# Optimization experiments

Measured on AMD Instinct MI355X. Metric: run time of the kernel, lower is better.

The kernel has to match this reference:

```python
import jax, jax.numpy as jnp
import numpy as np
from jax import lax

NUM_ITER = 40


def _pool(x, win, op, init):
    pads = [(0, 0), (0, 0)] + [(w // 2, w // 2) for w in win]
    return lax.reduce_window(x, init, op, (1, 1) + win, (1, 1, 1, 1, 1), pads)


def soft_erode(x):
    # -maxpool(-x) with zero-effect padding == min-pool padded with +inf.
    inf = jnp.asarray(jnp.inf, x.dtype)
    p1 = _pool(x, (3, 1, 1), lax.min, inf)
    p2 = _pool(x, (1, 3, 1), lax.min, inf)
    p3 = _pool(x, (1, 1, 3), lax.min, inf)
    return jnp.minimum(jnp.minimum(p1, p2), p3)


def soft_dilate(x):
    return _pool(x, (3, 3, 3), lax.max, jnp.asarray(-jnp.inf, x.dtype))


def soft_open(x):
    return soft_dilate(soft_erode(x))


def setup_inputs() -> dict:
    key = jax.random.key(0)
    img = jax.random.uniform(key, (2, 1, 192, 192, 192), dtype=jnp.float32)
    return {"img": img}


def reference(img):
    skeleton = jax.nn.relu(img - soft_open(img))

    def body(_, carry):
        im, skel = carry
        im = soft_erode(im)
        delta = jax.nn.relu(im - soft_open(im))
        skel = skel + jax.nn.relu(delta - skel * delta)
        return (im, skel)

    _, skeleton = lax.fori_loop(0, NUM_ITER, body, (img, skeleton))
    return skeleton
```

## Files before the change

### kernel.cpp

```cpp
#include <hip/hip_runtime.h>


#define Dn 192
#define Hn 192
#define Wn 192
#define PLANE (Hn * Wn)
#define TOTAL_ELEMS (2 * Dn * Hn * Wn)
#define NYG (Hn / 4)
#define ZPT 8
#define ZC (Dn / ZPT)
#define NBLK (NYG * ZC * 2)
#define NITER (ZPT + 4)

typedef _Float16 h2 __attribute__((ext_vector_type(2)));
typedef _Float16 h4 __attribute__((ext_vector_type(4)));

static __device__ __forceinline__ h2 h2min(h2 a, h2 b) { return __builtin_elementwise_min(a, b); }
static __device__ __forceinline__ h2 h2max(h2 a, h2 b) { return __builtin_elementwise_max(a, b); }
static __device__ __forceinline__ unsigned int u32(h2 v) { return __builtin_bit_cast(unsigned int, v); }
static __device__ __forceinline__ h2 h2c(unsigned int v) { return __builtin_bit_cast(h2, v); }

template <int CHUNK>
__device__ __forceinline__ int swizzle(int bid) {
    return (bid & 7) * CHUNK + (bid >> 3);
}

template <bool FIRST, bool LAST>
__global__ __launch_bounds__(192, 4) void step_k(const void* __restrict__ X_,
                                                 const _Float16* Sin,
                                                 void* Sout_,
                                                 _Float16* __restrict__ Aout) {
    const float* Xf = (const float*)X_;
    const _Float16* Xh = (const _Float16*)X_;
    _Float16* Sh = (_Float16*)Sout_;
    float* Sf = (float*)Sout_;

    const int bid = swizzle<NBLK / 8>((int)blockIdx.x);
    const int gy = bid % NYG;
    const int t2 = bid / NYG;
    const int zc = t2 % ZC;
    const int b = t2 / ZC;
    const int x = threadIdx.x;
    const int y0 = gy * 4;
    const int z0 = zc * ZPT;
    const int cbase = b * (Dn * PLANE) + y0 * Wn + x;

    int roff[8];
#pragma unroll
    for (int k = 0; k < 8; ++k) {
        int ry = y0 - 2 + k;
        ry = ry < 0 ? 0 : (ry > Hn - 1 ? Hn - 1 : ry);
        roff[k] = (ry - y0) * Wn;
    }

    __shared__ unsigned int sh[2][192][7];
    const int xu = (x < Wn - 1) ? x + 1 : x;
    const int xd = (x > 0) ? x - 1 : x;

    h2 aM2[3], aM1[3], hmM1[3], aUM1[3], aDM1[3];
    h2 xcM1[2], xcM2[2], e1cM1[2], mM1[2], mM2[2];

    _Float16 hP[8];
    float fP[8];
    h4 sP = {};

    auto issue = [&](int p) {
        int pz = p < 0 ? 0 : (p > Dn - 1 ? Dn - 1 : p);
        if (FIRST) {
            const float* pp = Xf + cbase + pz * PLANE;
#pragma unroll
            for (int k = 0; k < 8; ++k) fP[k] = pp[roff[k]];
        } else {
            const _Float16* pp = Xh + cbase + pz * PLANE;
#pragma unroll
            for (int k = 0; k < 8; ++k) hP[k] = pp[roff[k]];
        }
    };
    issue(z0 - 2);

#pragma unroll
    for (int i = 0; i < NITER; ++i) {
        const int p = z0 - 2 + i;
        const int zo = p - 2;

        _Float16 s[8];
#pragma unroll
        for (int k = 0; k < 8; ++k) s[k] = FIRST ? (_Float16)fP[k] : hP[k];

        if (i + 1 < NITER) issue(p + 1);

        h4 sN = {};
        if (!FIRST && i >= 3 && i + 1 < NITER) {
            const _Float16* sp = Sin + cbase + (p - 1) * PLANE;
            sN.x = sp[0]; sN.y = sp[Wn]; sN.z = sp[2 * Wn]; sN.w = sp[3 * Wn];
        }

        h2 P[7];
#pragma unroll
        for (int k = 0; k < 7; ++k) { h2 t = {s[k], s[k + 1]}; P[k] = t; }
        h2 a0[3] = {P[1], P[3], P[5]};
        h2 hm0[3];
#pragma unroll
        for (int j = 0; j < 3; ++j)
            hm0[j] = h2min(P[2 * j], h2min(P[2 * j + 1], P[2 * j + 2]));
        h2 xc0[2] = {P[2], P[4]};

        h2 e1[3];
        if (i >= 2) {
#pragma unroll
            for (int k = 0; k < 3; ++k)
                e1[k] = h2min(h2min(hmM1[k], aM2[k]),
                              h2min(h2min(aUM1[k], aDM1[k]), a0[k]));
            if (gy == 0)       e1[0] = __builtin_shufflevector(e1[0], e1[0], 1, 1);
            if (gy == NYG - 1) e1[2] = __builtin_shufflevector(e1[2], e1[2], 0, 0);
        }

        const int sl = i & 1;
        sh[sl][x][0] = u32(a0[0]);
        sh[sl][x][1] = u32(a0[1]);
        sh[sl][x][2] = u32(a0[2]);
        if (i >= 2) {
            sh[sl][x][3] = u32(e1[0]);
            sh[sl][x][4] = u32(e1[1]);
            sh[sl][x][5] = u32(e1[2]);
        }
        __syncthreads();
        h2 aU0[3] = {h2c(sh[sl][xu][0]), h2c(sh[sl][xu][1]), h2c(sh[sl][xu][2])};
        h2 aD0[3] = {h2c(sh[sl][xd][0]), h2c(sh[sl][xd][1]), h2c(sh[sl][xd][2])};

        h2 m0[2], e1c0[2];
        if (i >= 2) {
            h2 eU0 = h2c(sh[sl][xu][3]), eU1 = h2c(sh[sl][xu][4]), eU2 = h2c(sh[sl][xu][5]);
            h2 eD0 = h2c(sh[sl][xd][3]), eD1 = h2c(sh[sl][xd][4]), eD2 = h2c(sh[sl][xd][5]);
            h2 vm0 = h2max(e1[0], h2max(eU0, eD0));
            h2 vm1 = h2max(e1[1], h2max(eU1, eD1));
            h2 vm2 = h2max(e1[2], h2max(eU2, eD2));
            h2 mid01 = __builtin_shufflevector(vm0, vm1, 1, 2);
            h2 mid23 = __builtin_shufflevector(vm1, vm2, 1, 2);
            m0[0] = h2max(h2max(vm0, mid01), vm1);
            m0[1] = h2max(h2max(vm1, mid23), vm2);
            e1c0[0] = __builtin_shufflevector(e1[0], e1[1], 1, 2);
            e1c0[1] = __builtin_shufflevector(e1[1], e1[2], 1, 2);
        }

        if (i >= 4) {
            const int offo = cbase + zo * PLANE;
            const bool zlo = (zo == 0);
            const bool zhi = (zo == Dn - 1);
            h2 mzA0 = zlo ? mM1[0] : mM2[0];
            h2 mzA1 = zlo ? mM1[1] : mM2[1];
            h2 mzC0 = zhi ? mM1[0] : m0[0];
            h2 mzC1 = zhi ? mM1[1] : m0[1];
            h2 d01 = h2max(h2max(mzA0, mM1[0]), mzC0);
            h2 d23 = h2max(h2max(mzA1, mM1[1]), mzC1);

            float ex0 = (float)xcM2[0].x, ex1 = (float)xcM2[0].y;
            float ex2 = (float)xcM2[1].x, ex3 = (float)xcM2[1].y;
            float dl0 = (float)d01.x, dl1 = (float)d01.y;
            float dl2 = (float)d23.x, dl3 = (float)d23.y;
            float de0 = fmaxf(ex0 - dl0, 0.f);
            float de1 = fmaxf(ex1 - dl1, 0.f);
            float de2 = fmaxf(ex2 - dl2, 0.f);
            float de3 = fmaxf(ex3 - dl3, 0.f);
            float s0, s1, s2, s3;
            if (FIRST) {
                s0 = de0; s1 = de1; s2 = de2; s3 = de3;
            } else {
                s0 = (float)sP.x; s1 = (float)sP.y;
                s2 = (float)sP.z; s3 = (float)sP.w;
                s0 += fmaxf(de0 - s0 * de0, 0.f);
                s1 += fmaxf(de1 - s1 * de1, 0.f);
                s2 += fmaxf(de2 - s2 * de2, 0.f);
                s3 += fmaxf(de3 - s3 * de3, 0.f);
            }
            if (LAST) {
                Sf[offo] = s0; Sf[offo + Wn] = s1;
                Sf[offo + 2 * Wn] = s2; Sf[offo + 3 * Wn] = s3;
            } else {
                Sh[offo] = (_Float16)s0;
                Sh[offo + Wn] = (_Float16)s1;
                Sh[offo + 2 * Wn] = (_Float16)s2;
                Sh[offo + 3 * Wn] = (_Float16)s3;
                Aout[offo] = e1cM1[0].x;
                Aout[offo + Wn] = e1cM1[0].y;
                Aout[offo + 2 * Wn] = e1cM1[1].x;
                Aout[offo + 3 * Wn] = e1cM1[1].y;
            }
        }

#pragma unroll
        for (int k = 0; k < 3; ++k) {
            aM2[k] = aM1[k]; aM1[k] = a0[k];
            hmM1[k] = hm0[k]; aUM1[k] = aU0[k]; aDM1[k] = aD0[k];
        }
        xcM2[0] = xcM1[0]; xcM2[1] = xcM1[1];
        xcM1[0] = xc0[0];  xcM1[1] = xc0[1];
        if (i >= 2) {
            mM2[0] = mM1[0]; mM2[1] = mM1[1];
            mM1[0] = m0[0];  mM1[1] = m0[1];
            e1cM1[0] = e1c0[0]; e1cM1[1] = e1c0[1];
        }
        sP = sN;
    }
}

extern "C" void kernel_launch(void* const* d_in, const int* in_sizes, int n_in,
                              void* d_out, int out_size, void* d_ws, size_t ws_size,
                              hipStream_t stream) {
    const float* img = (const float*)d_in[0];
    _Float16* B0 = (_Float16*)d_ws;
    _Float16* B1 = B0 + TOTAL_ELEMS;
    _Float16* S  = B1 + TOTAL_ELEMS;

    step_k<true, false><<<NBLK, 192, 0, stream>>>(img, nullptr, S, B0);
    _Float16* a = B0;
    _Float16* nb = B1;
    for (int j = 1; j <= 39; ++j) {
        step_k<false, false><<<NBLK, 192, 0, stream>>>(a, S, S, nb);
        _Float16* t = a; a = nb; nb = t;
    }
    step_k<false, true><<<NBLK, 192, 0, stream>>>(a, S, d_out, nullptr);
}
```

Before: 1.123 ms.

## Fuse two skeleton iterations per kernel launch with wider halo

Adds a fused kernel that performs two erode/open/skeleton-update steps in one pass. It reads a 3-deep halo in z and y and keeps the second erosion's intermediates in registers and shared memory. This halves the number of launches and the global reads and writes of the eroded image and skeleton buffers. In exchange it adds redundant halo computation, more registers and larger shared memory per block. Min and max chains are also regrouped into three-input helpers.

Result: faster. 964.0 us (-14.2%).

```diff
diff --git a/kernel.cpp b/kernel.cpp
--- a/kernel.cpp
+++ b/kernel.cpp
@@ -10,19 +10,243 @@
 #define ZPT 8
 #define ZC (Dn / ZPT)
 #define NBLK (NYG * ZC * 2)
-#define NITER (ZPT + 4)
+#define NITER2 (ZPT + 6)
+#define NITER1 (ZPT + 4)
 
 typedef _Float16 h2 __attribute__((ext_vector_type(2)));
 typedef _Float16 h4 __attribute__((ext_vector_type(4)));
 
 static __device__ __forceinline__ h2 h2min(h2 a, h2 b) { return __builtin_elementwise_min(a, b); }
 static __device__ __forceinline__ h2 h2max(h2 a, h2 b) { return __builtin_elementwise_max(a, b); }
+static __device__ __forceinline__ h2 h2min3(h2 a, h2 b, h2 c) { return h2min(h2min(a, b), c); }
+static __device__ __forceinline__ h2 h2max3(h2 a, h2 b, h2 c) { return h2max(h2max(a, b), c); }
 static __device__ __forceinline__ unsigned int u32(h2 v) { return __builtin_bit_cast(unsigned int, v); }
 static __device__ __forceinline__ h2 h2c(unsigned int v) { return __builtin_bit_cast(h2, v); }
 
 template <int CHUNK>
 __device__ __forceinline__ int swizzle(int bid) {
     return (bid & 7) * CHUNK + (bid >> 3);
+}
+
+template <bool FIRST>
+__global__ __launch_bounds__(192, 4) void fused2_k(const void* __restrict__ X_,
+                                                   const _Float16* Sin,
+                                                   _Float16* Sout,
+                                                   _Float16* __restrict__ Aout) {
+    const float* Xf = (const float*)X_;
+    const _Float16* Xh = (const _Float16*)X_;
+
+    const int bid = swizzle<NBLK / 8>((int)blockIdx.x);
+    const int gy = bid % NYG;
+    const int t2 = bid / NYG;
+    const int zc = t2 % ZC;
+    const int b = t2 / ZC;
+    const int x = threadIdx.x;
+    const int y0 = gy * 4;
+    const int z0 = zc * ZPT;
+    const int cbase = b * (Dn * PLANE) + y0 * Wn + x;
+
+    int roff[10];
+#pragma unroll
+    for (int k = 0; k < 10; ++k) {
+        int ry = y0 - 3 + k;
+        ry = ry < 0 ? 0 : (ry > Hn - 1 ? Hn - 1 : ry);
+        roff[k] = (ry - y0) * Wn;
+    }
+
+    __shared__ unsigned int sh[2][192][11];
+    const int xu = (x < Wn - 1) ? x + 1 : x;
+    const int xd = (x > 0) ? x - 1 : x;
+
+    h2 aM1[4] = {}, aM2[4] = {}, hmM1[4] = {}, aUM1[4] = {}, aDM1[4] = {};
+    h2 e1M1t[3] = {}, e1M2t[3] = {}, hm1M1[3] = {}, e1UM1[3] = {}, e1DM1[3] = {};
+    h2 m1M1[2] = {}, m1M2[2] = {}, m1M3[2] = {};
+    h2 m2M1[2] = {}, m2M2[2] = {};
+    h2 xcM1[2] = {}, xcM2[2] = {}, xcM3[2] = {};
+    h2 e1cM1[2] = {}, e1cM2[2] = {}, e2cM1[2] = {};
+    h4 sP = {};
+
+    _Float16 hP[10];
+    float fP[10];
+    auto issue = [&](int p) {
+        int pz = p < 0 ? 0 : (p > Dn - 1 ? Dn - 1 : p);
+        if (FIRST) {
+            const float* pp = Xf + cbase + pz * PLANE;
+#pragma unroll
+            for (int k = 0; k < 10; ++k) fP[k] = pp[roff[k]];
+        } else {
+            const _Float16* pp = Xh + cbase + pz * PLANE;
+#pragma unroll
+            for (int k = 0; k < 10; ++k) hP[k] = pp[roff[k]];
+        }
+    };
+    issue(z0 - 3);
+
+#pragma unroll
+    for (int i = 0; i < NITER2; ++i) {
+        const int p = z0 - 3 + i;
+        const int zo = p - 3;
+
+        _Float16 s[10];
+#pragma unroll
+        for (int k = 0; k < 10; ++k) s[k] = FIRST ? (_Float16)fP[k] : hP[k];
+
+        if (i + 1 < NITER2) issue(p + 1);
+
+        h4 sN = {};
+        if (!FIRST && i >= 5 && i + 1 < NITER2) {
+            const _Float16* sp = Sin + cbase + (p - 2) * PLANE;
+            sN.x = sp[0]; sN.y = sp[Wn]; sN.z = sp[2 * Wn]; sN.w = sp[3 * Wn];
+        }
+
+        h2 P[9];
+#pragma unroll
+        for (int k = 0; k < 9; ++k) { h2 t = {s[k], s[k + 1]}; P[k] = t; }
+        h2 a0[4] = {P[1], P[3], P[5], P[7]};
+        h2 hm0[4];
+#pragma unroll
+        for (int j = 0; j < 4; ++j)
+            hm0[j] = h2min3(P[2 * j], P[2 * j + 1], P[2 * j + 2]);
+        h2 xc0[2] = {P[3], P[5]};
+
+        h2 e1[4] = {}, t[3] = {}, hm1_0[3] = {}, e1c0[2] = {};
+        if (i >= 2) {
+#pragma unroll
+            for (int k = 0; k < 4; ++k)
+                e1[k] = h2min3(h2min(hmM1[k], aM2[k]),
+                               h2min(aUM1[k], aDM1[k]), a0[k]);
+            if (gy == 0) { h2 v = {e1[1].x, e1[1].x}; e1[0] = v; }
+            if (gy == NYG - 1) { h2 v = {e1[2].y, e1[2].y}; e1[3] = v; }
+            t[0] = __builtin_shufflevector(e1[0], e1[1], 1, 2);
+            t[1] = __builtin_shufflevector(e1[1], e1[2], 1, 2);
+            t[2] = __builtin_shufflevector(e1[2], e1[3], 1, 2);
+            hm1_0[0] = h2min3(e1[0], t[0], e1[1]);
+            hm1_0[1] = h2min3(e1[1], t[1], e1[2]);
+            hm1_0[2] = h2min3(e1[2], t[2], e1[3]);
+            e1c0[0] = e1[1]; e1c0[1] = e1[2];
+        }
+
+        h2 e2[3] = {}, e2c0[2] = {};
+        if (i >= 4) {
+#pragma unroll
+            for (int j = 0; j < 3; ++j)
+                e2[j] = h2min3(h2min(hm1M1[j], e1M2t[j]),
+                               h2min(e1UM1[j], e1DM1[j]), t[j]);
+            if (gy == 0) { h2 v = {e2[0].y, e2[0].y}; e2[0] = v; }
+            if (gy == NYG - 1) { h2 v = {e2[2].x, e2[2].x}; e2[2] = v; }
+            e2c0[0] = __builtin_shufflevector(e2[0], e2[1], 1, 2);
+            e2c0[1] = __builtin_shufflevector(e2[1], e2[2], 1, 2);
+        }
+
+        const int sl = i & 1;
+#pragma unroll
+        for (int k = 0; k < 4; ++k) sh[sl][x][k] = u32(a0[k]);
+        if (i >= 2) {
+#pragma unroll
+            for (int j = 0; j < 3; ++j) sh[sl][x][4 + j] = u32(t[j]);
+        }
+        if (i >= 4) {
+#pragma unroll
+            for (int j = 0; j < 3; ++j) sh[sl][x][7 + j] = u32(e2[j]);
+        }
+        __syncthreads();
+        h2 aU0[4], aD0[4];
+#pragma unroll
+        for (int k = 0; k < 4; ++k) {
+            aU0[k] = h2c(sh[sl][xu][k]);
+            aD0[k] = h2c(sh[sl][xd][k]);
+        }
+        h2 tU[3] = {}, tD[3] = {}, m1_0[2] = {}, m2_0[2] = {};
+        if (i >= 2) {
+#pragma unroll
+            for (int j = 0; j < 3; ++j) {
+                tU[j] = h2c(sh[sl][xu][4 + j]);
+                tD[j] = h2c(sh[sl][xd][4 + j]);
+            }
+            h2 vm0 = h2max3(t[0], tU[0], tD[0]);
+            h2 vm1 = h2max3(t[1], tU[1], tD[1]);
+            h2 vm2 = h2max3(t[2], tU[2], tD[2]);
+            h2 mid01 = __builtin_shufflevector(vm0, vm1, 1, 2);
+            h2 mid23 = __builtin_shufflevector(vm1, vm2, 1, 2);
+            m1_0[0] = h2max3(vm0, mid01, vm1);
+            m1_0[1] = h2max3(vm1, mid23, vm2);
+        }
+        if (i >= 4) {
+            h2 eU0 = h2c(sh[sl][xu][7]), eU1 = h2c(sh[sl][xu][8]), eU2 = h2c(sh[sl][xu][9]);
+            h2 eD0 = h2c(sh[sl][xd][7]), eD1 = h2c(sh[sl][xd][8]), eD2 = h2c(sh[sl][xd][9]);
+            h2 vm0 = h2max3(e2[0], eU0, eD0);
+            h2 vm1 = h2max3(e2[1], eU1, eD1);
+            h2 vm2 = h2max3(e2[2], eU2, eD2);
+            h2 mid01 = __builtin_shufflevector(vm0, vm1, 1, 2);
+            h2 mid23 = __builtin_shufflevector(vm1, vm2, 1, 2);
+            m2_0[0] = h2max3(vm0, mid01, vm1);
+            m2_0[1] = h2max3(vm1, mid23, vm2);
+        }
+
+        if (i >= 6) {
+            const int offo = cbase + zo * PLANE;
+            const bool zlo = (zo == 0);
+            const bool zhi = (zo == Dn - 1);
+            h2 d1a0 = zlo ? m1M2[0] : m1M3[0];
+            h2 d1a1 = zlo ? m1M2[1] : m1M3[1];
+            h2 d1c0 = zhi ? m1M2[0] : m1M1[0];
+            h2 d1c1 = zhi ? m1M2[1] : m1M1[1];
+            h2 D1_0 = h2max3(d1a0, m1M2[0], d1c0);
+            h2 D1_1 = h2max3(d1a1, m1M2[1], d1c1);
+            h2 d2a0 = zlo ? m2M1[0] : m2M2[0];
+            h2 d2a1 = zlo ? m2M1[1] : m2M2[1];
+            h2 d2c0 = zhi ? m2M1[0] : m2_0[0];
+            h2 d2c1 = zhi ? m2M1[1] : m2_0[1];
+            h2 D2_0 = h2max3(d2a0, m2M1[0], d2c0);
+            h2 D2_1 = h2max3(d2a1, m2M1[1], d2c1);
+
+            float ex[4] = {(float)xcM3[0].x, (float)xcM3[0].y,
+                           (float)xcM3[1].x, (float)xcM3[1].y};
+            float e1v[4] = {(float)e1cM2[0].x, (float)e1cM2[0].y,
+                            (float)e1cM2[1].x, (float)e1cM2[1].y};
+            float d1[4] = {(float)D1_0.x, (float)D1_0.y, (float)D1_1.x, (float)D1_1.y};
+            float d2[4] = {(float)D2_0.x, (float)D2_0.y, (float)D2_1.x, (float)D2_1.y};
+            float sv[4] = {(float)sP.x, (float)sP.y, (float)sP.z, (float)sP.w};
+#pragma unroll
+            for (int q = 0; q < 4; ++q) {
+                float de1 = fmaxf(ex[q] - d1[q], 0.f);
+                float s1 = FIRST ? de1 : (sv[q] + fmaxf(de1 - sv[q] * de1, 0.f));
+                float de2 = fmaxf(e1v[q] - d2[q], 0.f);
+                sv[q] = s1 + fmaxf(de2 - s1 * de2, 0.f);
+            }
+            Sout[offo] = (_Float16)sv[0];
+            Sout[offo + Wn] = (_Float16)sv[1];
+            Sout[offo + 2 * Wn] = (_Float16)sv[2];
+            Sout[offo + 3 * Wn] = (_Float16)sv[3];
+            Aout[offo] = e2cM1[0].x;
+            Aout[offo + Wn] = e2cM1[0].y;
+            Aout[offo + 2 * Wn] = e2cM1[1].x;
+            Aout[offo + 3 * Wn] = e2cM1[1].y;
+        }
+
+#pragma unroll
+        for (int k = 0; k < 4; ++k) {
+            aM2[k] = aM1[k]; aM1[k] = a0[k];
+            hmM1[k] = hm0[k]; aUM1[k] = aU0[k]; aDM1[k] = aD0[k];
+        }
+#pragma unroll
+        for (int j = 0; j < 3; ++j) {
+            e1M2t[j] = e1M1t[j]; e1M1t[j] = t[j];
+            hm1M1[j] = hm1_0[j]; e1UM1[j] = tU[j]; e1DM1[j] = tD[j];
+        }
+        m1M3[0] = m1M2[0]; m1M3[1] = m1M2[1];
+        m1M2[0] = m1M1[0]; m1M2[1] = m1M1[1];
+        m1M1[0] = m1_0[0]; m1M1[1] = m1_0[1];
+        m2M2[0] = m2M1[0]; m2M2[1] = m2M1[1];
+        m2M1[0] = m2_0[0]; m2M1[1] = m2_0[1];
+        xcM3[0] = xcM2[0]; xcM3[1] = xcM2[1];
+        xcM2[0] = xcM1[0]; xcM2[1] = xcM1[1];
+        xcM1[0] = xc0[0];  xcM1[1] = xc0[1];
+        e1cM2[0] = e1cM1[0]; e1cM2[1] = e1cM1[1];
+        e1cM1[0] = e1c0[0]; e1cM1[1] = e1c0[1];
+        e2cM1[0] = e2c0[0]; e2cM1[1] = e2c0[1];
+        sP = sN;
+    }
 }
 
 template <bool FIRST, bool LAST>
@@ -79,7 +303,7 @@
     issue(z0 - 2);
 
 #pragma unroll
-    for (int i = 0; i < NITER; ++i) {
+    for (int i = 0; i < NITER1; ++i) {
         const int p = z0 - 2 + i;
         const int zo = p - 2;
 
@@ -87,10 +311,10 @@
 #pragma unroll
         for (int k = 0; k < 8; ++k) s[k] = FIRST ? (_Float16)fP[k] : hP[k];
 
-        if (i + 1 < NITER) issue(p + 1);
+        if (i + 1 < NITER1) issue(p + 1);
 
         h4 sN = {};
-        if (!FIRST && i >= 3 && i + 1 < NITER) {
+        if (!FIRST && i >= 3 && i + 1 < NITER1) {
             const _Float16* sp = Sin + cbase + (p - 1) * PLANE;
             sN.x = sp[0]; sN.y = sp[Wn]; sN.z = sp[2 * Wn]; sN.w = sp[3 * Wn];
         }
@@ -102,15 +326,15 @@
         h2 hm0[3];
 #pragma unroll
         for (int j = 0; j < 3; ++j)
-            hm0[j] = h2min(P[2 * j], h2min(P[2 * j + 1], P[2 * j + 2]));
+            hm0[j] = h2min3(P[2 * j], P[2 * j + 1], P[2 * j + 2]);
         h2 xc0[2] = {P[2], P[4]};
 
         h2 e1[3];
         if (i >= 2) {
 #pragma unroll
             for (int k = 0; k < 3; ++k)
-                e1[k] = h2min(h2min(hmM1[k], aM2[k]),
-                              h2min(h2min(aUM1[k], aDM1[k]), a0[k]));
+                e1[k] = h2min3(h2min(hmM1[k], aM2[k]),
+                               h2min(aUM1[k], aDM1[k]), a0[k]);
             if (gy == 0)       e1[0] = __builtin_shufflevector(e1[0], e1[0], 1, 1);
             if (gy == NYG - 1) e1[2] = __builtin_shufflevector(e1[2], e1[2], 0, 0);
         }
@@ -132,13 +356,13 @@
         if (i >= 2) {
             h2 eU0 = h2c(sh[sl][xu][3]), eU1 = h2c(sh[sl][xu][4]), eU2 = h2c(sh[sl][xu][5]);
             h2 eD0 = h2c(sh[sl][xd][3]), eD1 = h2c(sh[sl][xd][4]), eD2 = h2c(sh[sl][xd][5]);
-            h2 vm0 = h2max(e1[0], h2max(eU0, eD0));
-            h2 vm1 = h2max(e1[1], h2max(eU1, eD1));
-            h2 vm2 = h2max(e1[2], h2max(eU2, eD2));
+            h2 vm0 = h2max3(e1[0], eU0, eD0);
+            h2 vm1 = h2max3(e1[1], eU1, eD1);
+            h2 vm2 = h2max3(e1[2], eU2, eD2);
             h2 mid01 = __builtin_shufflevector(vm0, vm1, 1, 2);
             h2 mid23 = __builtin_shufflevector(vm1, vm2, 1, 2);
-            m0[0] = h2max(h2max(vm0, mid01), vm1);
-            m0[1] = h2max(h2max(vm1, mid23), vm2);
+            m0[0] = h2max3(vm0, mid01, vm1);
+            m0[1] = h2max3(vm1, mid23, vm2);
             e1c0[0] = __builtin_shufflevector(e1[0], e1[1], 1, 2);
             e1c0[1] = __builtin_shufflevector(e1[1], e1[2], 1, 2);
         }
@@ -151,17 +375,15 @@
             h2 mzA1 = zlo ? mM1[1] : mM2[1];
             h2 mzC0 = zhi ? mM1[0] : m0[0];
             h2 mzC1 = zhi ? mM1[1] : m0[1];
-            h2 d01 = h2max(h2max(mzA0, mM1[0]), mzC0);
-            h2 d23 = h2max(h2max(mzA1, mM1[1]), mzC1);
+            h2 d01 = h2max3(mzA0, mM1[0], mzC0);
+            h2 d23 = h2max3(mzA1, mM1[1], mzC1);
 
             float ex0 = (float)xcM2[0].x, ex1 = (float)xcM2[0].y;
             float ex2 = (float)xcM2[1].x, ex3 = (float)xcM2[1].y;
-            float dl0 = (float)d01.x, dl1 = (float)d01.y;
-            float dl2 = (float)d23.x, dl3 = (float)d23.y;
-            float de0 = fmaxf(ex0 - dl0, 0.f);
-            float de1 = fmaxf(ex1 - dl1, 0.f);
-            float de2 = fmaxf(ex2 - dl2, 0.f);
-            float de3 = fmaxf(ex3 - dl3, 0.f);
+            float de0 = fmaxf(ex0 - (float)d01.x, 0.f);
+            float de1 = fmaxf(ex1 - (float)d01.y, 0.f);
+            float de2 = fmaxf(ex2 - (float)d23.x, 0.f);
+            float de3 = fmaxf(ex3 - (float)d23.y, 0.f);
             float s0, s1, s2, s3;
             if (FIRST) {
                 s0 = de0; s1 = de1; s2 = de2; s3 = de3;
@@ -212,11 +434,11 @@
     _Float16* B1 = B0 + TOTAL_ELEMS;
     _Float16* S  = B1 + TOTAL_ELEMS;
 
-    step_k<true, false><<<NBLK, 192, 0, stream>>>(img, nullptr, S, B0);
+    fused2_k<true><<<NBLK, 192, 0, stream>>>(img, nullptr, S, B0);
     _Float16* a = B0;
     _Float16* nb = B1;
-    for (int j = 1; j <= 39; ++j) {
-        step_k<false, false><<<NBLK, 192, 0, stream>>>(a, S, S, nb);
+    for (int j = 0; j < 19; ++j) {
+        fused2_k<false><<<NBLK, 192, 0, stream>>>(a, S, S, nb);
         _Float16* t = a; a = nb; nb = t;
     }
     step_k<false, true><<<NBLK, 192, 0, stream>>>(a, S, d_out, nullptr);
```
